# Performance work log

Measured on AMD Instinct MI355X. Metric: run time of the kernel, lower is better.

Reference implementation:

```python
import jax, jax.numpy as jnp
import numpy as np
import math

B, T, N_CTX, H = 4, 512, 2048, 1024
NUM_HEADS, NUM_INSTRUMENTS, MAX_BARS = 16, 16, 8
HEAD_DIM = H // NUM_HEADS


def setup_inputs() -> dict:
    key = jax.random.key(0)
    ks = jax.random.split(key, 16)
    s = 1.0 / math.sqrt(H)
    return {
        "query": jax.random.normal(ks[0], (B, T, H), jnp.float32),
        "context": jax.random.normal(ks[1], (B, N_CTX, H), jnp.float32),
        "instrument_ids": jax.random.randint(ks[2], (B, N_CTX), 0, NUM_INSTRUMENTS),
        "current_instrument_id": 3,
        "bar_offsets": jax.random.randint(ks[3], (B, N_CTX), 0, MAX_BARS),
        "Wq": jax.random.normal(ks[4], (H, H), jnp.float32) * s,
        "bq": jnp.zeros((H,), jnp.float32),
        "Wk": jax.random.normal(ks[5], (H, H), jnp.float32) * s,
        "bk": jnp.zeros((H,), jnp.float32),
        "Wv": jax.random.normal(ks[6], (H, H), jnp.float32) * s,
        "bv": jnp.zeros((H,), jnp.float32),
        "Wo": jax.random.normal(ks[7], (H, H), jnp.float32) * s,
        "bo": jnp.zeros((H,), jnp.float32),
        "inst_emb": jax.random.normal(ks[8], (NUM_INSTRUMENTS, H), jnp.float32),
        "bar_emb": jax.random.normal(ks[9], (MAX_BARS, H), jnp.float32),
    }


def reference(query, context, instrument_ids, current_instrument_id, bar_offsets,
              Wq, bq, Wk, bk, Wv, bv, Wo, bo, inst_emb, bar_emb):
    # current_instrument_id: python int -> broadcast to (B,)
    cur = jnp.full((B,), current_instrument_id, dtype=jnp.int64 if instrument_ids.dtype == jnp.int64 else jnp.int32)
    # add embeddings to query and context
    q = query + inst_emb[cur][:, None, :]                              # (B,T,H)
    ctx = context + inst_emb[instrument_ids] + bar_emb[jnp.clip(bar_offsets, 0, MAX_BARS - 1)]  # (B,N,H)
    # projections (torch Linear: x @ W.T + b)
    Q = (q @ Wq.T + bq).reshape(B, T, NUM_HEADS, HEAD_DIM).transpose(0, 2, 1, 3)      # (B,h,T,d)
    K = (ctx @ Wk.T + bk).reshape(B, N_CTX, NUM_HEADS, HEAD_DIM).transpose(0, 2, 1, 3)  # (B,h,N,d)
    V = (ctx @ Wv.T + bv).reshape(B, N_CTX, NUM_HEADS, HEAD_DIM).transpose(0, 2, 1, 3)  # (B,h,N,d)
    scores = jnp.einsum('bhtd,bhnd->bhtn', Q, K) / math.sqrt(HEAD_DIM)  # (B,h,T,N)
    # attend only to keys whose instrument differs from the current one
    keep = (instrument_ids != cur[:, None])[:, None, None, :]           # (B,1,1,N)
    scores = jnp.where(keep, scores, jnp.float32(-1e9))
    probs = jax.nn.softmax(scores, axis=-1)
    out = jnp.einsum('bhtn,bhnd->bhtd', probs, V).transpose(0, 2, 1, 3).reshape(B, T, H)
    return out @ Wo.T + bo
```

## Files before the change

### kernel.cpp

```cpp
#include <hip/hip_runtime.h>

#define H 1024
#define B_ 4
#define T_ 512
#define NCTX 2048
#define NH 16
#define HD 64

typedef __attribute__((ext_vector_type(8))) short bf16x8;
typedef __attribute__((ext_vector_type(4))) float f32x4;
typedef __attribute__((ext_vector_type(4))) short s16x4;

__device__ __forceinline__ ushort f2b(float f) {
  union { float f; unsigned u; } v; v.f = f;
  unsigned u = v.u;
  unsigned r = (u + 0x7FFFu + ((u >> 16) & 1u)) >> 16;
  return (ushort)r;
}

__device__ __forceinline__ unsigned cvt_pk_bf16(float lo, float hi) {
  unsigned r;
  asm("v_cvt_pk_bf16_f32 %0, %1, %2" : "=v"(r) : "v"(lo), "v"(hi));
  return r;
}

__device__ __forceinline__ void gld16(const void* g, void* l) {
  __builtin_amdgcn_global_load_lds((const __attribute__((address_space(1))) unsigned int*)g,
                                   (__attribute__((address_space(3))) unsigned int*)l, 16, 0, 0);
}


__global__ void prep_all(const float* __restrict__ query, const float* __restrict__ ctx,
                         const int* __restrict__ ids, const int* __restrict__ curp,
                         const int* __restrict__ bars,
                         const float* __restrict__ iemb, const float* __restrict__ bemb,
                         const float* __restrict__ Wq, const float* __restrict__ Wk,
                         const float* __restrict__ Wv, const float* __restrict__ Wo,
                         ushort* __restrict__ qin, ushort* __restrict__ ctxb,
                         ushort* __restrict__ Wqb, ushort* __restrict__ Wkb,
                         ushort* __restrict__ Wvb, ushort* __restrict__ Wob,
                         float* __restrict__ maskf) {
  int blk = blockIdx.x;
  if (blk < 8192) {
    int i = blk * 256 + threadIdx.x;
    int row = i >> 8;
    int c4 = i & 255;
    int id = ids[row];
    int bar = bars[row];
    bar = bar < 0 ? 0 : (bar > 7 ? 7 : bar);
    float4 v = ((const float4*)ctx)[i];
    float4 e = ((const float4*)(iemb + (size_t)id * H))[c4];
    float4 g = ((const float4*)(bemb + (size_t)bar * H))[c4];
    s16x4 o;
    o[0] = (short)f2b(v.x + e.x + g.x); o[1] = (short)f2b(v.y + e.y + g.y);
    o[2] = (short)f2b(v.z + e.z + g.z); o[3] = (short)f2b(v.w + e.w + g.w);
    ((s16x4*)ctxb)[i] = o;
  } else if (blk < 10240) {
    int cur = curp[0];
    int i = (blk - 8192) * 256 + threadIdx.x;
    int c4 = i & 255;
    float4 v = ((const float4*)query)[i];
    float4 e = ((const float4*)(iemb + (size_t)cur * H))[c4];
    s16x4 o;
    o[0] = (short)f2b(v.x + e.x); o[1] = (short)f2b(v.y + e.y);
    o[2] = (short)f2b(v.z + e.z); o[3] = (short)f2b(v.w + e.w);
    ((s16x4*)qin)[i] = o;
  } else if (blk < 14336) {
    int b2 = blk - 10240;
    int which = b2 >> 10;
    int i = (b2 & 1023) * 256 + threadIdx.x;
    const float* s = which == 0 ? Wq : which == 1 ? Wk : which == 2 ? Wv : Wo;
    ushort* d = which == 0 ? Wqb : which == 1 ? Wkb : which == 2 ? Wvb : Wob;
    float4 v = ((const float4*)s)[i];
    s16x4 o;
    o[0] = (short)f2b(v.x); o[1] = (short)f2b(v.y);
    o[2] = (short)f2b(v.z); o[3] = (short)f2b(v.w);
    ((s16x4*)d)[i] = o;
  } else {
    int cur = curp[0];
    int i = (blk - 14336) * 256 + threadIdx.x;
    maskf[i] = (ids[i] != cur) ? 0.f : -1e30f;
  }
}


__global__ __launch_bounds__(256) void proj_k(const ushort* __restrict__ Aq,
                                              const ushort* __restrict__ Actx,
                                              const ushort* __restrict__ WQ,
                                              const ushort* __restrict__ WK,
                                              const ushort* __restrict__ WV,
                                              const float* __restrict__ bQ,
                                              const float* __restrict__ bK,
                                              const float* __restrict__ bV,
                                              ushort* __restrict__ Qout,
                                              ushort* __restrict__ Kout,
                                              ushort* __restrict__ VTout) {
  const int id = blockIdx.x;
  const ushort* A;
  const ushort* W;
  const float* bias;
  int row0, col0, mode;
  ushort* Cout;
  if (id < 1024) {
    int xcd = id & 7, rest = id >> 3;
    int bx = rest & 15, by = (rest >> 4) * 8 + xcd;
    A = Actx; row0 = by * 128;
    if (bx < 8) { W = WK; bias = bK; col0 = bx * 128; mode = 0; Cout = Kout; }
    else        { W = WV; bias = bV; col0 = (bx - 8) * 128; mode = 1; Cout = VTout; }
  } else {
    int q = id - 1024;
    A = Aq; row0 = (q >> 3) * 128; col0 = (q & 7) * 128;
    W = WQ; bias = bQ; mode = 2; Cout = Qout;
  }

  __shared__ ushort As[2][128 * 32];
  __shared__ ushort Bs[2][128 * 32];
  const int tid = threadIdx.x;
  const int lane = tid & 63;
  const int wv = tid >> 6;
  const int wr = wv >> 1, wc = wv & 1;
  const int lo = lane & 15, hi = lane >> 4;

  f32x4 acc[4][4];
#pragma unroll
  for (int m = 0; m < 4; m++)
#pragma unroll
    for (int n = 0; n < 4; n++) acc[m][n] = (f32x4){0.f, 0.f, 0.f, 0.f};

#pragma unroll
  for (int c = 0; c < 2; c++) {
    int ia = wv * 128 + c * 64 + lane;
    int r = ia >> 2, s = ia & 3;
    gld16(A + (size_t)(row0 + r) * H + s * 8, (char*)As[0] + (wv * 128 + c * 64) * 16);
    gld16(W + (size_t)(col0 + r) * H + s * 8, (char*)Bs[0] + (wv * 128 + c * 64) * 16);
  }
  __syncthreads();

  int cur = 0;
  for (int kt = 0; kt < 32; kt++) {
    if (kt < 31) {
#pragma unroll
      for (int c = 0; c < 2; c++) {
        int ia = wv * 128 + c * 64 + lane;
        int r = ia >> 2, s = ia & 3;
        gld16(A + (size_t)(row0 + r) * H + (kt + 1) * 32 + s * 8,
              (char*)As[cur ^ 1] + (wv * 128 + c * 64) * 16);
        gld16(W + (size_t)(col0 + r) * H + (kt + 1) * 32 + s * 8,
              (char*)Bs[cur ^ 1] + (wv * 128 + c * 64) * 16);
      }
    }
    bf16x8 af[4], bfr[4];
#pragma unroll
    for (int m = 0; m < 4; m++) af[m] = *(const bf16x8*)(As[cur] + (wr * 64 + m * 16 + lo) * 32 + hi * 8);
#pragma unroll
    for (int n = 0; n < 4; n++) bfr[n] = *(const bf16x8*)(Bs[cur] + (wc * 64 + n * 16 + lo) * 32 + hi * 8);
#pragma unroll
    for (int m = 0; m < 4; m++)
#pragma unroll
      for (int n = 0; n < 4; n++)
        acc[m][n] = __builtin_amdgcn_mfma_f32_16x16x32_bf16(af[m], bfr[n], acc[m][n], 0, 0, 0);
    __syncthreads();
    cur ^= 1;
  }

#pragma unroll
  for (int m = 0; m < 4; m++) {
    int gr0 = row0 + wr * 64 + m * 16 + hi * 4;
#pragma unroll
    for (int n = 0; n < 4; n++) {
      int gc = col0 + wc * 64 + n * 16 + lo;
      float bv = bias[gc];
      if (mode == 0) {
#pragma unroll
        for (int r = 0; r < 4; r++)
          Cout[(size_t)(gr0 + r) * H + gc] = f2b(acc[m][n][r] + bv);
      } else if (mode == 1) {
        int bb = gr0 >> 11, n0 = gr0 & 2047;
        s16x4 o;
#pragma unroll
        for (int r = 0; r < 4; r++) o[r] = (short)f2b(acc[m][n][r] + bv);
        *(s16x4*)(Cout + (size_t)bb * (H * NCTX) + (size_t)gc * NCTX + n0) = o;
      } else {
#pragma unroll
        for (int r = 0; r < 4; r++)
          Cout[(size_t)(gr0 + r) * H + gc] = f2b((acc[m][n][r] + bv) * 0.125f);
      }
    }
  }
}


__global__ __launch_bounds__(256) void gemm_o(const ushort* __restrict__ A,
                                              const ushort* __restrict__ W,
                                              const float* __restrict__ bias,
                                              float* __restrict__ Cout) {
  __shared__ ushort As[2][128 * 32];
  __shared__ ushort Bs[2][128 * 32];
  const int tid = threadIdx.x;
  const int lane = tid & 63;
  const int wv = tid >> 6;
  const int wr = wv >> 1, wc = wv & 1;
  const int lo = lane & 15, hi = lane >> 4;
  const int row0 = blockIdx.y * 128, col0 = blockIdx.x * 128;

  f32x4 acc[4][4];
#pragma unroll
  for (int m = 0; m < 4; m++)
#pragma unroll
    for (int n = 0; n < 4; n++) acc[m][n] = (f32x4){0.f, 0.f, 0.f, 0.f};

#pragma unroll
  for (int c = 0; c < 2; c++) {
    int ia = wv * 128 + c * 64 + lane;
    int r = ia >> 2, s = ia & 3;
    gld16(A + (size_t)(row0 + r) * H + s * 8, (char*)As[0] + (wv * 128 + c * 64) * 16);
    gld16(W + (size_t)(col0 + r) * H + s * 8, (char*)Bs[0] + (wv * 128 + c * 64) * 16);
  }
  __syncthreads();

  int cur = 0;
  for (int kt = 0; kt < 32; kt++) {
    if (kt < 31) {
#pragma unroll
      for (int c = 0; c < 2; c++) {
        int ia = wv * 128 + c * 64 + lane;
        int r = ia >> 2, s = ia & 3;
        gld16(A + (size_t)(row0 + r) * H + (kt + 1) * 32 + s * 8,
              (char*)As[cur ^ 1] + (wv * 128 + c * 64) * 16);
        gld16(W + (size_t)(col0 + r) * H + (kt + 1) * 32 + s * 8,
              (char*)Bs[cur ^ 1] + (wv * 128 + c * 64) * 16);
      }
    }
    bf16x8 af[4], bfr[4];
#pragma unroll
    for (int m = 0; m < 4; m++) af[m] = *(const bf16x8*)(As[cur] + (wr * 64 + m * 16 + lo) * 32 + hi * 8);
#pragma unroll
    for (int n = 0; n < 4; n++) bfr[n] = *(const bf16x8*)(Bs[cur] + (wc * 64 + n * 16 + lo) * 32 + hi * 8);
#pragma unroll
    for (int m = 0; m < 4; m++)
#pragma unroll
      for (int n = 0; n < 4; n++)
        acc[m][n] = __builtin_amdgcn_mfma_f32_16x16x32_bf16(af[m], bfr[n], acc[m][n], 0, 0, 0);
    __syncthreads();
    cur ^= 1;
  }

#pragma unroll
  for (int m = 0; m < 4; m++) {
    int gr0 = row0 + wr * 64 + m * 16 + hi * 4;
#pragma unroll
    for (int n = 0; n < 4; n++) {
      int gc = col0 + wc * 64 + n * 16 + lo;
      float bv = bias[gc];
#pragma unroll
      for (int r = 0; r < 4; r++)
        Cout[(size_t)(gr0 + r) * H + gc] = acc[m][n][r] + bv;
    }
  }
}


#define NSPLIT 2
#define KVLEN (NCTX / NSPLIT)
#define NT_KV (KVLEN / 64)

__global__ __launch_bounds__(256) void attn_k(const ushort* __restrict__ Q,
                                              const ushort* __restrict__ K,
                                              const ushort* __restrict__ VT,
                                              const float* __restrict__ maskf,
                                              float* __restrict__ OPf,
                                              float* __restrict__ mlf) {
  __shared__ ushort Ks[2][64 * 64];
  __shared__ ushort Vs[2][64 * 64];
  __shared__ ushort Ps[4][16 * 64];
  const int blk = (blockIdx.x & 7) * 128 + (blockIdx.x >> 3);
  const int qt = blk & 7;
  const int h = (blk >> 3) & 15;
  const int b = (blk >> 7) & 3;
  const int p = blk >> 9;
  const int tid = threadIdx.x, lane = tid & 63, w = tid >> 6;
  const int lo = lane & 15, hi = lane >> 4;
  const int swz = (lo & 7) << 4;
  const int kvbase = p * KVLEN;

  const ushort* Qp = Q + ((size_t)(b * T_ + qt * 64 + w * 16 + lo)) * H + h * HD;
  bf16x8 qf0 = *(const bf16x8*)(Qp + hi * 8);
  bf16x8 qf1 = *(const bf16x8*)(Qp + 32 + hi * 8);

  f32x4 oacc[4];
#pragma unroll
  for (int d = 0; d < 4; d++) oacc[d] = (f32x4){0.f, 0.f, 0.f, 0.f};
  float mrow = -1e30f, lrow = 0.f;

  const float* maskb = maskf + b * NCTX;
  const ushort* Kbase = K + ((size_t)(b * NCTX)) * H + h * HD;
  const ushort* Vbase = VT + (size_t)b * (H * NCTX) + (size_t)(h * HD) * NCTX;

  bf16x8 kr[2], vr[2];
#pragma unroll
  for (int i = 0; i < 2; i++) {
    int seg = tid + i * 256;
    int r = seg >> 3, s = seg & 7;
    kr[i] = *(const bf16x8*)(Kbase + (size_t)(kvbase + r) * H + s * 8);
    vr[i] = *(const bf16x8*)(Vbase + (size_t)r * NCTX + kvbase + s * 8);
  }
#pragma unroll
  for (int i = 0; i < 2; i++) {
    int seg = tid + i * 256;
    int r = seg >> 3, s = seg & 7;
    int wb = (r * 128 + s * 16) ^ ((r & 7) << 4);
    *(bf16x8*)((char*)Ks[0] + wb) = kr[i];
    *(bf16x8*)((char*)Vs[0] + wb) = vr[i];
  }
  __syncthreads();

  int curbuf = 0;
  for (int t = 0; t < NT_KV; t++) {
    int kvt = kvbase + t * 64;
    if (t < NT_KV - 1) {
#pragma unroll
      for (int i = 0; i < 2; i++) {
        int seg = tid + i * 256;
        int r = seg >> 3, s = seg & 7;
        kr[i] = *(const bf16x8*)(Kbase + (size_t)(kvt + 64 + r) * H + s * 8);
        vr[i] = *(const bf16x8*)(Vbase + (size_t)r * NCTX + kvt + 64 + s * 8);
      }
    }

    f32x4 sc[4];
    __builtin_amdgcn_s_setprio(1);
#pragma unroll
    for (int nt = 0; nt < 4; nt++) {
      bf16x8 kf0 = *(const bf16x8*)((char*)Ks[curbuf] + ((((nt * 16 + lo) * 128) + hi * 16) ^ swz));
      bf16x8 kf1 = *(const bf16x8*)((char*)Ks[curbuf] + ((((nt * 16 + lo) * 128) + 64 + hi * 16) ^ swz));
      f32x4 z = (f32x4){0.f, 0.f, 0.f, 0.f};
      z = __builtin_amdgcn_mfma_f32_16x16x32_bf16(kf0, qf0, z, 0, 0, 0);
      sc[nt] = __builtin_amdgcn_mfma_f32_16x16x32_bf16(kf1, qf1, z, 0, 0, 0);
    }
    __builtin_amdgcn_s_setprio(0);

    float pv[4][4];
#pragma unroll
    for (int nt = 0; nt < 4; nt++) {
      float4 mv = *(const float4*)(maskb + kvt + nt * 16 + hi * 4);
      pv[nt][0] = sc[nt][0] + mv.x;
      pv[nt][1] = sc[nt][1] + mv.y;
      pv[nt][2] = sc[nt][2] + mv.z;
      pv[nt][3] = sc[nt][3] + mv.w;
    }

    float m0 = fmaxf(fmaxf(pv[0][0], pv[0][1]), fmaxf(pv[0][2], pv[0][3]));
    float m1 = fmaxf(fmaxf(pv[1][0], pv[1][1]), fmaxf(pv[1][2], pv[1][3]));
    float m2 = fmaxf(fmaxf(pv[2][0], pv[2][1]), fmaxf(pv[2][2], pv[2][3]));
    float m3 = fmaxf(fmaxf(pv[3][0], pv[3][1]), fmaxf(pv[3][2], pv[3][3]));
    float x = fmaxf(fmaxf(m0, m1), fmaxf(m2, m3));
    x = fmaxf(x, __shfl_xor(x, 16));
    x = fmaxf(x, __shfl_xor(x, 32));
    bool defer = __all((x <= mrow + 8.0f) && (mrow > -1e29f));
    float mn, scal = 1.f;
    if (defer) {
      mn = mrow;
    } else {
      mn = fmaxf(mrow, x);
      scal = __expf(mrow - mn);
      mrow = mn;
    }
    float rsp[4];
#pragma unroll
    for (int nt = 0; nt < 4; nt++) {
      float e0 = __expf(pv[nt][0] - mn);
      float e1 = __expf(pv[nt][1] - mn);
      float e2 = __expf(pv[nt][2] - mn);
      float e3 = __expf(pv[nt][3] - mn);
      pv[nt][0] = e0; pv[nt][1] = e1; pv[nt][2] = e2; pv[nt][3] = e3;
      rsp[nt] = (e0 + e1) + (e2 + e3);
    }
    float rs = (rsp[0] + rsp[1]) + (rsp[2] + rsp[3]);
    rs += __shfl_xor(rs, 16);
    rs += __shfl_xor(rs, 32);
    if (defer) {
      lrow += rs;
    } else {
      lrow = lrow * scal + rs;
      float sq0 = __shfl(scal, hi * 4 + 0);
      float sq1 = __shfl(scal, hi * 4 + 1);
      float sq2 = __shfl(scal, hi * 4 + 2);
      float sq3 = __shfl(scal, hi * 4 + 3);
#pragma unroll
      for (int d = 0; d < 4; d++) {
        oacc[d][0] *= sq0; oacc[d][1] *= sq1; oacc[d][2] *= sq2; oacc[d][3] *= sq3;
      }
    }

#pragma unroll
    for (int nt = 0; nt < 4; nt++) {
      uint2 pw;
      pw.x = cvt_pk_bf16(pv[nt][0], pv[nt][1]);
      pw.y = cvt_pk_bf16(pv[nt][2], pv[nt][3]);
      *(uint2*)((char*)Ps[w] + ((lo * 128 + (nt * 16 + hi * 4) * 2) ^ swz)) = pw;
    }

    __builtin_amdgcn_s_setprio(1);
#pragma unroll
    for (int ks = 0; ks < 2; ks++) {
      bf16x8 pa = *(const bf16x8*)((char*)Ps[w] + ((lo * 128 + (ks * 64 + hi * 16)) ^ swz));
#pragma unroll
      for (int d = 0; d < 4; d++) {
        bf16x8 vf = *(const bf16x8*)((char*)Vs[curbuf] + (((d * 16 + lo) * 128 + ks * 64 + hi * 16) ^ swz));
        oacc[d] = __builtin_amdgcn_mfma_f32_16x16x32_bf16(pa, vf, oacc[d], 0, 0, 0);
      }
    }
    __builtin_amdgcn_s_setprio(0);

    if (t < NT_KV - 1) {
#pragma unroll
      for (int i = 0; i < 2; i++) {
        int seg = tid + i * 256;
        int r = seg >> 3, s = seg & 7;
        int wb = (r * 128 + s * 16) ^ ((r & 7) << 4);
        *(bf16x8*)((char*)Ks[curbuf ^ 1] + wb) = kr[i];
        *(bf16x8*)((char*)Vs[curbuf ^ 1] + wb) = vr[i];
      }
    }
    __syncthreads();
    curbuf ^= 1;
  }

  int row0 = b * 512 + qt * 64 + w * 16 + hi * 4;
#pragma unroll
  for (int d = 0; d < 4; d++) {
#pragma unroll
    for (int r = 0; r < 4; r++)
      OPf[((size_t)p * 2048 + row0 + r) * 1024 + h * 64 + d * 16 + lo] = oacc[d][r];
  }
  if (hi == 0) {
    int qrow = b * 512 + qt * 64 + w * 16 + lo;
    mlf[(((size_t)p * 2048 + qrow) * 16 + h) * 2] = mrow;
    mlf[(((size_t)p * 2048 + qrow) * 16 + h) * 2 + 1] = lrow;
  }
}

__global__ void attn_combine(const float* __restrict__ OPf, const float* __restrict__ mlf,
                             ushort* __restrict__ O) {
  int idx = blockIdx.x * 256 + threadIdx.x;
  int btr = idx >> 8;
  int c4 = idx & 255;
  int h = c4 >> 4;
  float m0 = mlf[((size_t)btr * 16 + h) * 2];
  float l0 = mlf[((size_t)btr * 16 + h) * 2 + 1];
  float m1 = mlf[(((size_t)2048 + btr) * 16 + h) * 2];
  float l1 = mlf[(((size_t)2048 + btr) * 16 + h) * 2 + 1];
  float M = fmaxf(m0, m1);
  float a0 = __expf(m0 - M), a1 = __expf(m1 - M);
  float inv = 1.0f / (a0 * l0 + a1 * l1);
  float4 o0 = ((const float4*)OPf)[idx];
  float4 o1 = ((const float4*)OPf)[(size_t)524288 + idx];
  s16x4 r;
  r[0] = (short)f2b((a0 * o0.x + a1 * o1.x) * inv);
  r[1] = (short)f2b((a0 * o0.y + a1 * o1.y) * inv);
  r[2] = (short)f2b((a0 * o0.z + a1 * o1.z) * inv);
  r[3] = (short)f2b((a0 * o0.w + a1 * o1.w) * inv);
  ((s16x4*)O)[idx] = r;
}


extern "C" void kernel_launch(void* const* d_in, const int* in_sizes, int n_in,
                              void* d_out, int out_size, void* d_ws, size_t ws_size,
                              hipStream_t stream) {
  const float* query = (const float*)d_in[0];
  const float* context = (const float*)d_in[1];
  const int* ids = (const int*)d_in[2];
  const int* curp = (const int*)d_in[3];
  const int* bars = (const int*)d_in[4];
  const float* Wq = (const float*)d_in[5];
  const float* bq = (const float*)d_in[6];
  const float* Wk = (const float*)d_in[7];
  const float* bk = (const float*)d_in[8];
  const float* Wv = (const float*)d_in[9];
  const float* bv = (const float*)d_in[10];
  const float* Wo = (const float*)d_in[11];
  const float* bo = (const float*)d_in[12];
  const float* iemb = (const float*)d_in[13];
  const float* bemb = (const float*)d_in[14];
  float* out = (float*)d_out;

  ushort* ws = (ushort*)d_ws;
  ushort* Wqb = ws;
  ushort* Wkb = Wqb + (1u << 20);
  ushort* Wvb = Wkb + (1u << 20);
  ushort* Wob = Wvb + (1u << 20);
  ushort* qin = Wob + (1u << 20);
  ushort* ctxb = qin + (2u << 20);
  ushort* Qb = ctxb + (8u << 20);
  ushort* Kb = Qb + (2u << 20);
  ushort* VTb = Kb + (8u << 20);
  ushort* AOb = VTb + (8u << 20);

  float* OPf = (float*)ctxb;
  float* mlf = (float*)qin;
  float* maskf = out;

  prep_all<<<14368, 256, 0, stream>>>(query, context, ids, curp, bars, iemb, bemb,
                                      Wq, Wk, Wv, Wo, qin, ctxb, Wqb, Wkb, Wvb, Wob, maskf);

  proj_k<<<1152, 256, 0, stream>>>(qin, ctxb, Wqb, Wkb, Wvb, bq, bk, bv, Qb, Kb, VTb);

  attn_k<<<1024, 256, 0, stream>>>(Qb, Kb, VTb, maskf, OPf, mlf);
  attn_combine<<<2048, 256, 0, stream>>>(OPf, mlf, AOb);

  gemm_o<<<dim3(8, 16), 256, 0, stream>>>(AOb, Wob, bo, out);
}
```

Measured before the change: 159.6 us.

## Swizzle GEMM LDS tiles and single-buffer attention K/V shared memory

Both GEMM kernels now XOR-swizzle the 16-byte column segment by row, applied on the global-to-LDS load address and on the fragment reads, to cut LDS bank conflicts on the MFMA operand loads. The attention kernel drops its double-buffered K/V LDS tiles in favour of one buffer. Register-staged prefetch is kept, and a second barrier is added before the LDS writes. This halves K/V LDS use, which may raise occupancy, but it adds an extra sync per KV tile.

```diff
diff --git a/kernel.cpp b/kernel.cpp
--- a/kernel.cpp
+++ b/kernel.cpp
@@ -131,8 +131,9 @@
   for (int c = 0; c < 2; c++) {
     int ia = wv * 128 + c * 64 + lane;
     int r = ia >> 2, s = ia & 3;
-    gld16(A + (size_t)(row0 + r) * H + s * 8, (char*)As[0] + (wv * 128 + c * 64) * 16);
-    gld16(W + (size_t)(col0 + r) * H + s * 8, (char*)Bs[0] + (wv * 128 + c * 64) * 16);
+    int sg = s ^ (r & 3);
+    gld16(A + (size_t)(row0 + r) * H + sg * 8, (char*)As[0] + (wv * 128 + c * 64) * 16);
+    gld16(W + (size_t)(col0 + r) * H + sg * 8, (char*)Bs[0] + (wv * 128 + c * 64) * 16);
   }
   __syncthreads();
 
@@ -143,17 +144,24 @@
       for (int c = 0; c < 2; c++) {
         int ia = wv * 128 + c * 64 + lane;
         int r = ia >> 2, s = ia & 3;
-        gld16(A + (size_t)(row0 + r) * H + (kt + 1) * 32 + s * 8,
+        int sg = s ^ (r & 3);
+        gld16(A + (size_t)(row0 + r) * H + (kt + 1) * 32 + sg * 8,
               (char*)As[cur ^ 1] + (wv * 128 + c * 64) * 16);
-        gld16(W + (size_t)(col0 + r) * H + (kt + 1) * 32 + s * 8,
+        gld16(W + (size_t)(col0 + r) * H + (kt + 1) * 32 + sg * 8,
               (char*)Bs[cur ^ 1] + (wv * 128 + c * 64) * 16);
       }
     }
     bf16x8 af[4], bfr[4];
 #pragma unroll
-    for (int m = 0; m < 4; m++) af[m] = *(const bf16x8*)(As[cur] + (wr * 64 + m * 16 + lo) * 32 + hi * 8);
-#pragma unroll
-    for (int n = 0; n < 4; n++) bfr[n] = *(const bf16x8*)(Bs[cur] + (wc * 64 + n * 16 + lo) * 32 + hi * 8);
+    for (int m = 0; m < 4; m++) {
+      int rr = wr * 64 + m * 16 + lo;
+      af[m] = *(const bf16x8*)(As[cur] + rr * 32 + (hi ^ (rr & 3)) * 8);
+    }
+#pragma unroll
+    for (int n = 0; n < 4; n++) {
+      int rr = wc * 64 + n * 16 + lo;
+      bfr[n] = *(const bf16x8*)(Bs[cur] + rr * 32 + (hi ^ (rr & 3)) * 8);
+    }
 #pragma unroll
     for (int m = 0; m < 4; m++)
 #pragma unroll
@@ -213,8 +221,9 @@
   for (int c = 0; c < 2; c++) {
     int ia = wv * 128 + c * 64 + lane;
     int r = ia >> 2, s = ia & 3;
-    gld16(A + (size_t)(row0 + r) * H + s * 8, (char*)As[0] + (wv * 128 + c * 64) * 16);
-    gld16(W + (size_t)(col0 + r) * H + s * 8, (char*)Bs[0] + (wv * 128 + c * 64) * 16);
+    int sg = s ^ (r & 3);
+    gld16(A + (size_t)(row0 + r) * H + sg * 8, (char*)As[0] + (wv * 128 + c * 64) * 16);
+    gld16(W + (size_t)(col0 + r) * H + sg * 8, (char*)Bs[0] + (wv * 128 + c * 64) * 16);
   }
   __syncthreads();
 
@@ -225,17 +234,24 @@
       for (int c = 0; c < 2; c++) {
         int ia = wv * 128 + c * 64 + lane;
         int r = ia >> 2, s = ia & 3;
-        gld16(A + (size_t)(row0 + r) * H + (kt + 1) * 32 + s * 8,
+        int sg = s ^ (r & 3);
+        gld16(A + (size_t)(row0 + r) * H + (kt + 1) * 32 + sg * 8,
               (char*)As[cur ^ 1] + (wv * 128 + c * 64) * 16);
-        gld16(W + (size_t)(col0 + r) * H + (kt + 1) * 32 + s * 8,
+        gld16(W + (size_t)(col0 + r) * H + (kt + 1) * 32 + sg * 8,
               (char*)Bs[cur ^ 1] + (wv * 128 + c * 64) * 16);
       }
     }
     bf16x8 af[4], bfr[4];
 #pragma unroll
-    for (int m = 0; m < 4; m++) af[m] = *(const bf16x8*)(As[cur] + (wr * 64 + m * 16 + lo) * 32 + hi * 8);
-#pragma unroll
-    for (int n = 0; n < 4; n++) bfr[n] = *(const bf16x8*)(Bs[cur] + (wc * 64 + n * 16 + lo) * 32 + hi * 8);
+    for (int m = 0; m < 4; m++) {
+      int rr = wr * 64 + m * 16 + lo;
+      af[m] = *(const bf16x8*)(As[cur] + rr * 32 + (hi ^ (rr & 3)) * 8);
+    }
+#pragma unroll
+    for (int n = 0; n < 4; n++) {
+      int rr = wc * 64 + n * 16 + lo;
+      bfr[n] = *(const bf16x8*)(Bs[cur] + rr * 32 + (hi ^ (rr & 3)) * 8);
+    }
 #pragma unroll
     for (int m = 0; m < 4; m++)
 #pragma unroll
@@ -270,8 +286,8 @@
                                               const float* __restrict__ maskf,
                                               float* __restrict__ OPf,
                                               float* __restrict__ mlf) {
-  __shared__ ushort Ks[2][64 * 64];
-  __shared__ ushort Vs[2][64 * 64];
+  __shared__ ushort Ks[64 * 64];
+  __shared__ ushort Vs[64 * 64];
   __shared__ ushort Ps[4][16 * 64];
   const int blk = (blockIdx.x & 7) * 128 + (blockIdx.x >> 3);
   const int qt = blk & 7;
@@ -296,43 +312,37 @@
   const ushort* Kbase = K + ((size_t)(b * NCTX)) * H + h * HD;
   const ushort* Vbase = VT + (size_t)b * (H * NCTX) + (size_t)(h * HD) * NCTX;
 
-  bf16x8 kr[2], vr[2];
-#pragma unroll
-  for (int i = 0; i < 2; i++) {
-    int seg = tid + i * 256;
-    int r = seg >> 3, s = seg & 7;
-    kr[i] = *(const bf16x8*)(Kbase + (size_t)(kvbase + r) * H + s * 8);
-    vr[i] = *(const bf16x8*)(Vbase + (size_t)r * NCTX + kvbase + s * 8);
-  }
-#pragma unroll
-  for (int i = 0; i < 2; i++) {
-    int seg = tid + i * 256;
-    int r = seg >> 3, s = seg & 7;
-    int wb = (r * 128 + s * 16) ^ ((r & 7) << 4);
-    *(bf16x8*)((char*)Ks[0] + wb) = kr[i];
-    *(bf16x8*)((char*)Vs[0] + wb) = vr[i];
-  }
+  const int sr = tid >> 3, ss = tid & 7;
+  const int wb0 = (sr * 128 + ss * 16) ^ ((sr & 7) << 4);
+  const int sr1 = (tid + 256) >> 3, ss1 = (tid + 256) & 7;
+  const int wb1 = (sr1 * 128 + ss1 * 16) ^ ((sr1 & 7) << 4);
+
+  bf16x8 kr0, kr1, vr0, vr1;
+  kr0 = *(const bf16x8*)(Kbase + (size_t)(kvbase + sr) * H + ss * 8);
+  vr0 = *(const bf16x8*)(Vbase + (size_t)sr * NCTX + kvbase + ss * 8);
+  kr1 = *(const bf16x8*)(Kbase + (size_t)(kvbase + sr1) * H + ss1 * 8);
+  vr1 = *(const bf16x8*)(Vbase + (size_t)sr1 * NCTX + kvbase + ss1 * 8);
+  *(bf16x8*)((char*)Ks + wb0) = kr0;
+  *(bf16x8*)((char*)Vs + wb0) = vr0;
+  *(bf16x8*)((char*)Ks + wb1) = kr1;
+  *(bf16x8*)((char*)Vs + wb1) = vr1;
   __syncthreads();
 
-  int curbuf = 0;
   for (int t = 0; t < NT_KV; t++) {
     int kvt = kvbase + t * 64;
     if (t < NT_KV - 1) {
-#pragma unroll
-      for (int i = 0; i < 2; i++) {
-        int seg = tid + i * 256;
-        int r = seg >> 3, s = seg & 7;
-        kr[i] = *(const bf16x8*)(Kbase + (size_t)(kvt + 64 + r) * H + s * 8);
-        vr[i] = *(const bf16x8*)(Vbase + (size_t)r * NCTX + kvt + 64 + s * 8);
-      }
+      kr0 = *(const bf16x8*)(Kbase + (size_t)(kvt + 64 + sr) * H + ss * 8);
+      vr0 = *(const bf16x8*)(Vbase + (size_t)sr * NCTX + kvt + 64 + ss * 8);
+      kr1 = *(const bf16x8*)(Kbase + (size_t)(kvt + 64 + sr1) * H + ss1 * 8);
+      vr1 = *(const bf16x8*)(Vbase + (size_t)sr1 * NCTX + kvt + 64 + ss1 * 8);
     }
 
     f32x4 sc[4];
     __builtin_amdgcn_s_setprio(1);
 #pragma unroll
     for (int nt = 0; nt < 4; nt++) {
-      bf16x8 kf0 = *(const bf16x8*)((char*)Ks[curbuf] + ((((nt * 16 + lo) * 128) + hi * 16) ^ swz));
-      bf16x8 kf1 = *(const bf16x8*)((char*)Ks[curbuf] + ((((nt * 16 + lo) * 128) + 64 + hi * 16) ^ swz));
+      bf16x8 kf0 = *(const bf16x8*)((char*)Ks + ((((nt * 16 + lo) * 128) + hi * 16) ^ swz));
+      bf16x8 kf1 = *(const bf16x8*)((char*)Ks + ((((nt * 16 + lo) * 128) + 64 + hi * 16) ^ swz));
       f32x4 z = (f32x4){0.f, 0.f, 0.f, 0.f};
       z = __builtin_amdgcn_mfma_f32_16x16x32_bf16(kf0, qf0, z, 0, 0, 0);
       sc[nt] = __builtin_amdgcn_mfma_f32_16x16x32_bf16(kf1, qf1, z, 0, 0, 0);
@@ -406,24 +416,20 @@
       bf16x8 pa = *(const bf16x8*)((char*)Ps[w] + ((lo * 128 + (ks * 64 + hi * 16)) ^ swz));
 #pragma unroll
       for (int d = 0; d < 4; d++) {
-        bf16x8 vf = *(const bf16x8*)((char*)Vs[curbuf] + (((d * 16 + lo) * 128 + ks * 64 + hi * 16) ^ swz));
+        bf16x8 vf = *(const bf16x8*)((char*)Vs + (((d * 16 + lo) * 128 + ks * 64 + hi * 16) ^ swz));
         oacc[d] = __builtin_amdgcn_mfma_f32_16x16x32_bf16(pa, vf, oacc[d], 0, 0, 0);
       }
     }
     __builtin_amdgcn_s_setprio(0);
 
     if (t < NT_KV - 1) {
-#pragma unroll
-      for (int i = 0; i < 2; i++) {
-        int seg = tid + i * 256;
-        int r = seg >> 3, s = seg & 7;
-        int wb = (r * 128 + s * 16) ^ ((r & 7) << 4);
-        *(bf16x8*)((char*)Ks[curbuf ^ 1] + wb) = kr[i];
-        *(bf16x8*)((char*)Vs[curbuf ^ 1] + wb) = vr[i];
-      }
-    }
-    __syncthreads();
-    curbuf ^= 1;
+      __syncthreads();
+      *(bf16x8*)((char*)Ks + wb0) = kr0;
+      *(bf16x8*)((char*)Vs + wb0) = vr0;
+      *(bf16x8*)((char*)Ks + wb1) = kr1;
+      *(bf16x8*)((char*)Vs + wb1) = vr1;
+      __syncthreads();
+    }
   }
 
   int row0 = b * 512 + qt * 64 + w * 16 + hi * 4;
```

New measurement: 160.8 us. About the same (+0.7%).
